# Optimization experiments

Hardware: AMD Instinct MI355X
Metric: run time of the kernel (lower is better)

## Reference

```python
import jax, jax.numpy as jnp
import numpy as np

IN_FEATURES = 512
NUM_CASES = 64
N_POINTS = 131072
HIDDEN = 512
OUT_FEATURES = 512


def _wn_linear(x, V, g, b):
    # torch weight_norm with dim=0 on Linear weight [out, in]: per-row norm over in-dim
    W = V * (g / jnp.linalg.norm(V, axis=1))[:, None]
    return x @ W.T + b


def _consolidative_matmul(mask, x):
    # group-by-caseID mean pooling expressed as masked matmul (matches torch forward)
    sel_sum = jnp.sum(mask, axis=-1, keepdims=True)
    sel_sum = jnp.maximum(sel_sum, 1.0)  # relu(s-1)+1 == max(s,1) for s>=0
    return (mask @ x) / sel_sum


def setup_inputs() -> dict:
    key = jax.random.key(0)
    ks = jax.random.split(key, 8)
    feat = jax.random.normal(ks[0], (N_POINTS, IN_FEATURES), dtype=jnp.float32)
    cid = jax.random.randint(ks[1], (N_POINTS, 1), 0, NUM_CASES).astype(jnp.float32)
    x = jnp.concatenate([feat, cid], axis=-1)  # [N, 513]
    s = 0.05
    V0 = jax.random.normal(ks[2], (HIDDEN, IN_FEATURES), dtype=jnp.float32) * s
    g0 = jnp.ones((HIDDEN,), dtype=jnp.float32)
    b0 = jnp.zeros((HIDDEN,), dtype=jnp.float32)
    V1 = jax.random.normal(ks[3], (HIDDEN, HIDDEN), dtype=jnp.float32) * s
    g1 = jnp.ones((HIDDEN,), dtype=jnp.float32)
    b1 = jnp.zeros((HIDDEN,), dtype=jnp.float32)
    Wf = jax.random.normal(ks[4], (OUT_FEATURES, HIDDEN), dtype=jnp.float32) * s
    bf = jnp.zeros((OUT_FEATURES,), dtype=jnp.float32)
    return {"x": x, "V0": V0, "g0": g0, "b0": b0,
            "V1": V1, "g1": g1, "b1": b1, "Wf": Wf, "bf": bf}


def reference(x, V0, g0, b0, V1, g1, b1, Wf, bf):
    feat = x[..., :IN_FEATURES]                    # [N, 512]
    cid = jax.lax.stop_gradient(x[..., IN_FEATURES:IN_FEATURES + 1])  # [N, 1]
    case_range = jnp.arange(NUM_CASES, dtype=x.dtype)[:, None]        # [C, 1]
    d = jnp.swapaxes(cid, -1, -2) - case_range     # [C, N]
    # Unit_function: 1 iff -0.5 < d < 0.5, else 0 (hard, zero-grad)
    mask = jnp.where((d > -0.5) & (d < 0.5), 1.0, 0.0).astype(x.dtype)
    mask = jax.lax.stop_gradient(mask)
    h = _consolidative_matmul(mask, feat)          # [C, 512] per-case mean
    h = jax.nn.silu(_wn_linear(h, V0, g0, b0))
    h = jax.nn.silu(_wn_linear(h, V1, g1, b1))
    h = h @ Wf.T + bf                              # final layer, identity activation
    out = jnp.swapaxes(mask, -1, -2) @ h           # scatter-back combine [N, 512]
    return out
```

## Files before the change

### kernel.cpp

```cpp
#include <hip/hip_runtime.h>
#include <math.h>

#define NPTS   131072
#define INF    512
#define ROWF   513
#define NCASE  64
#define HID    512
#define NB     256
#define CHUNK  512
#define SEG    16

__global__ __launch_bounds__(256)
void k_hist(const float* __restrict__ x, int* __restrict__ hist,
            int* __restrict__ cids) {
  __shared__ int h[NCASE];
  const int t = threadIdx.x;
  const int b = blockIdx.x;
  if (t < NCASE) h[t] = 0;
  __syncthreads();
  const int base = b * CHUNK;
  for (int i = t; i < CHUNK; i += 256) {
    float cf = x[(size_t)(base + i) * ROWF + INF];
    int c = (int)(cf + 0.5f);
    cids[base + i] = c;
    atomicAdd(&h[c], 1);
  }
  __syncthreads();
  if (t < NCASE) hist[b * NCASE + t] = h[t];
}

__global__ __launch_bounds__(64)
void k_scan(const int* __restrict__ hist, int* __restrict__ rel,
            int* __restrict__ base, int* __restrict__ cnt,
            float* __restrict__ cntf) {
  __shared__ int lcnt[NCASE];
  __shared__ int lbase[NCASE];
  const int c = threadIdx.x;
  int running = 0;
  for (int b = 0; b < NB; ++b) {
    rel[b * NCASE + c] = running;
    running += hist[b * NCASE + c];
  }
  lcnt[c] = running;
  cnt[c] = running;
  cntf[c] = (float)running;
  __syncthreads();
  if (c == 0) {
    int acc = 0;
    for (int i = 0; i < NCASE; ++i) { lbase[i] = acc; acc += lcnt[i]; }
  }
  __syncthreads();
  base[c] = lbase[c];
}

__global__ __launch_bounds__(64)
void k_build(const int* __restrict__ cids, const int* __restrict__ rel,
             const int* __restrict__ base, int* __restrict__ idxlist) {
  __shared__ int cidl[CHUNK];
  const int lane = threadIdx.x;
  const int b = blockIdx.x;
  for (int i = lane; i < CHUNK; i += 64) cidl[i] = cids[b * CHUNK + i];
  __syncthreads();
  int myoff = rel[b * NCASE + lane] + base[lane];
  int rank = 0;
  for (int i = 0; i < CHUNK; ++i) {
    if (cidl[i] == lane) { idxlist[myoff + rank] = b * CHUNK + i; ++rank; }
  }
}

__global__ __launch_bounds__(128)
void k_sum(const float* __restrict__ x, const int* __restrict__ idxlist,
           const int* __restrict__ base, const int* __restrict__ cnt,
           float* __restrict__ psum) {
  const int t = threadIdx.x;
  const int s = blockIdx.x;
  const int c = blockIdx.y;
  const int n = cnt[c];
  const int bs = base[c];
  int p0 = (s * n) / SEG;
  int p1 = ((s + 1) * n) / SEG;

  float a0 = 0.f, a1 = 0.f, a2 = 0.f, a3 = 0.f;
  int p = p0;
  for (; p + 4 <= p1; p += 4) {
    int i0 = __builtin_amdgcn_readfirstlane(idxlist[bs + p + 0]);
    int i1 = __builtin_amdgcn_readfirstlane(idxlist[bs + p + 1]);
    int i2 = __builtin_amdgcn_readfirstlane(idxlist[bs + p + 2]);
    int i3 = __builtin_amdgcn_readfirstlane(idxlist[bs + p + 3]);
    const float* r0 = x + (size_t)i0 * ROWF + t;
    const float* r1 = x + (size_t)i1 * ROWF + t;
    const float* r2 = x + (size_t)i2 * ROWF + t;
    const float* r3 = x + (size_t)i3 * ROWF + t;
    float v00 = r0[0], v01 = r0[128], v02 = r0[256], v03 = r0[384];
    float v10 = r1[0], v11 = r1[128], v12 = r1[256], v13 = r1[384];
    float v20 = r2[0], v21 = r2[128], v22 = r2[256], v23 = r2[384];
    float v30 = r3[0], v31 = r3[128], v32 = r3[256], v33 = r3[384];
    a0 += v00; a1 += v01; a2 += v02; a3 += v03;
    a0 += v10; a1 += v11; a2 += v12; a3 += v13;
    a0 += v20; a1 += v21; a2 += v22; a3 += v23;
    a0 += v30; a1 += v31; a2 += v32; a3 += v33;
  }
  for (; p < p1; ++p) {
    int i0 = __builtin_amdgcn_readfirstlane(idxlist[bs + p]);
    const float* r0 = x + (size_t)i0 * ROWF + t;
    a0 += r0[0]; a1 += r0[128]; a2 += r0[256]; a3 += r0[384];
  }
  float* od = psum + ((size_t)c * SEG + s) * HID;
  od[t] = a0; od[t + 128] = a1; od[t + 256] = a2; od[t + 384] = a3;
}

__global__ __launch_bounds__(512)
void k_h0(const float* __restrict__ psum, const float* __restrict__ cntf,
          float* __restrict__ h0) {
  const int c = blockIdx.x;
  const int f = threadIdx.x;
  float s = 0.f;
  for (int seg = 0; seg < SEG; ++seg) s += psum[((size_t)c * SEG + seg) * HID + f];
  h0[(size_t)c * HID + f] = s / fmaxf(cntf[c], 1.f);
}

__global__ __launch_bounds__(256)
void k_scale(const float* __restrict__ V, const float* __restrict__ g,
             float* __restrict__ scale, int K) {
  __shared__ float red[256];
  const int row = blockIdx.x;
  const int t   = threadIdx.x;
  const float* vr = V + (size_t)row * K;
  float s = 0.f;
  for (int k = t; k < K; k += 256) { float v = vr[k]; s += v * v; }
  red[t] = s;
  __syncthreads();
  for (int w = 128; w > 0; w >>= 1) {
    if (t < w) red[t] += red[t + w];
    __syncthreads();
  }
  if (t == 0) scale[row] = g[row] / sqrtf(red[0]);
}

template <bool SILU, bool SCALED>
__global__ __launch_bounds__(256)
void k_layer(const float* __restrict__ hin, const float* __restrict__ W,
             const float* __restrict__ scale, const float* __restrict__ bias,
             float* __restrict__ hout) {
  const int n = blockIdx.y;
  const int o = blockIdx.x * 256 + threadIdx.x;
  const float* hr = hin + (size_t)n * HID;
  const float* wr = W + (size_t)o * HID;
  float s0 = 0.f, s1 = 0.f, s2 = 0.f, s3 = 0.f;
  for (int k = 0; k < HID; k += 4) {
    s0 += hr[k + 0] * wr[k + 0];
    s1 += hr[k + 1] * wr[k + 1];
    s2 += hr[k + 2] * wr[k + 2];
    s3 += hr[k + 3] * wr[k + 3];
  }
  float s = (s0 + s1) + (s2 + s3);
  float y = SCALED ? (s * scale[o] + bias[o]) : (s + bias[o]);
  if (SILU) y = y / (1.f + expf(-y));
  hout[(size_t)n * HID + o] = y;
}

__global__ __launch_bounds__(256)
void k_scatter(const int* __restrict__ idxlist, const int* __restrict__ base,
               const int* __restrict__ cnt, const float* __restrict__ h3,
               float* __restrict__ out) {
  const int t = threadIdx.x;
  const int s = blockIdx.x;
  const int c = blockIdx.y;
  const int n = cnt[c];
  const int bs = base[c];
  int p0 = (s * n) / SEG;
  int p1 = ((s + 1) * n) / SEG;
  const int q = t & 127;
  const int which = t >> 7;
  float4 hv = ((const float4*)(h3 + (size_t)c * HID))[q];
  for (int p = p0 + which; p < p1; p += 2) {
    int idx = __builtin_amdgcn_readfirstlane(idxlist[bs + p]);
    ((float4*)(out + (size_t)idx * HID))[q] = hv;
  }
}

extern "C" void kernel_launch(void* const* d_in, const int* in_sizes, int n_in,
                              void* d_out, int out_size, void* d_ws, size_t ws_size,
                              hipStream_t stream) {
  const float* x  = (const float*)d_in[0];
  const float* V0 = (const float*)d_in[1];
  const float* g0 = (const float*)d_in[2];
  const float* b0 = (const float*)d_in[3];
  const float* V1 = (const float*)d_in[4];
  const float* g1 = (const float*)d_in[5];
  const float* b1 = (const float*)d_in[6];
  const float* Wf = (const float*)d_in[7];
  const float* bf = (const float*)d_in[8];
  float* out = (float*)d_out;
  float* ws  = (float*)d_ws;

  size_t off = 0;
  float* psum   = ws + off; off += (size_t)NCASE * SEG * HID;
  float* h0     = ws + off; off += NCASE * HID;
  float* h1     = ws + off; off += NCASE * HID;
  float* h2     = ws + off; off += NCASE * HID;
  float* h3     = ws + off; off += NCASE * HID;
  float* scale0 = ws + off; off += 512;
  float* scale1 = ws + off; off += 512;
  float* cntf   = ws + off; off += 64;
  int* iws = (int*)(ws + off);
  size_t ioff = 0;
  int* hist    = iws + ioff; ioff += NB * NCASE;
  int* rel     = iws + ioff; ioff += NB * NCASE;
  int* basec   = iws + ioff; ioff += NCASE;
  int* cnt     = iws + ioff; ioff += NCASE;
  int* cids    = iws + ioff; ioff += NPTS;
  int* idxlist = iws + ioff; ioff += NPTS;

  k_hist <<<dim3(NB), dim3(256), 0, stream>>>(x, hist, cids);
  k_scan <<<dim3(1), dim3(64), 0, stream>>>(hist, rel, basec, cnt, cntf);
  k_build<<<dim3(NB), dim3(64), 0, stream>>>(cids, rel, basec, idxlist);
  k_sum  <<<dim3(SEG, NCASE), dim3(128), 0, stream>>>(x, idxlist, basec, cnt, psum);
  k_h0   <<<dim3(NCASE), dim3(512), 0, stream>>>(psum, cntf, h0);
  k_scale<<<dim3(512), dim3(256), 0, stream>>>(V0, g0, scale0, HID);
  k_scale<<<dim3(512), dim3(256), 0, stream>>>(V1, g1, scale1, HID);
  k_layer<true,  true ><<<dim3(2, NCASE), dim3(256), 0, stream>>>(h0, V0, scale0, b0, h1);
  k_layer<true,  true ><<<dim3(2, NCASE), dim3(256), 0, stream>>>(h1, V1, scale1, b1, h2);
  k_layer<false, false><<<dim3(2, NCASE), dim3(256), 0, stream>>>(h2, Wf, nullptr, bf, h3);
  k_scatter<<<dim3(SEG, NCASE), dim3(256), 0, stream>>>(idxlist, basec, cnt, h3, out);
}
```

Measured before the change: 235.4 us.

## Parallelize scan, fuse reductions and scales, and scatter by point order

Replaces the serial single-block scan with a 64-block parallel Hillis-Steele scan over a transposed histogram. The per-case base offsets are recomputed with wave shuffles inside the consumer kernels. The two weight-norm scale kernels are merged into one, and the segment reduce (h0) is folded into the first layer kernel, which also stages its input row in shared memory. k_sum doubles its segment count and unrolls by 8. The scatter now walks points in order and writes contiguous output rows instead of gathering per case, aiming for coalesced stores. The aim is fewer launches, less serial latency and better memory access patterns. Costs are redundant per-block prefix sums and the segment reduction being repeated in both column blocks of layer 1.

```diff
diff --git a/kernel.cpp b/kernel.cpp
--- a/kernel.cpp
+++ b/kernel.cpp
@@ -8,7 +8,7 @@
 #define HID    512
 #define NB     256
 #define CHUNK  512
-#define SEG    16
+#define SEG    32
 
 __global__ __launch_bounds__(256)
 void k_hist(const float* __restrict__ x, int* __restrict__ hist,
@@ -26,42 +26,44 @@
     atomicAdd(&h[c], 1);
   }
   __syncthreads();
-  if (t < NCASE) hist[b * NCASE + t] = h[t];
-}
-
-__global__ __launch_bounds__(64)
+  if (t < NCASE) hist[t * NB + b] = h[t];
+}
+
+__global__ __launch_bounds__(256)
 void k_scan(const int* __restrict__ hist, int* __restrict__ rel,
-            int* __restrict__ base, int* __restrict__ cnt,
-            float* __restrict__ cntf) {
-  __shared__ int lcnt[NCASE];
-  __shared__ int lbase[NCASE];
-  const int c = threadIdx.x;
-  int running = 0;
-  for (int b = 0; b < NB; ++b) {
-    rel[b * NCASE + c] = running;
-    running += hist[b * NCASE + c];
-  }
-  lcnt[c] = running;
-  cnt[c] = running;
-  cntf[c] = (float)running;
-  __syncthreads();
-  if (c == 0) {
-    int acc = 0;
-    for (int i = 0; i < NCASE; ++i) { lbase[i] = acc; acc += lcnt[i]; }
-  }
-  __syncthreads();
-  base[c] = lbase[c];
+            int* __restrict__ cnt) {
+  __shared__ int buf[NB];
+  const int c = blockIdx.x;
+  const int t = threadIdx.x;
+  const int v = hist[c * NB + t];
+  buf[t] = v;
+  __syncthreads();
+  for (int d = 1; d < NB; d <<= 1) {
+    int u = (t >= d) ? buf[t - d] : 0;
+    __syncthreads();
+    buf[t] += u;
+    __syncthreads();
+  }
+  rel[t * NCASE + c] = buf[t] - v;
+  if (t == NB - 1) cnt[c] = buf[t];
 }
 
 __global__ __launch_bounds__(64)
 void k_build(const int* __restrict__ cids, const int* __restrict__ rel,
-             const int* __restrict__ base, int* __restrict__ idxlist) {
+             const int* __restrict__ cnt, int* __restrict__ idxlist) {
   __shared__ int cidl[CHUNK];
   const int lane = threadIdx.x;
   const int b = blockIdx.x;
   for (int i = lane; i < CHUNK; i += 64) cidl[i] = cids[b * CHUNK + i];
-  __syncthreads();
-  int myoff = rel[b * NCASE + lane] + base[lane];
+  int lv = cnt[lane];
+  int sc = lv;
+  for (int d = 1; d < 64; d <<= 1) {
+    int u = __shfl_up(sc, d, 64);
+    if (lane >= d) sc += u;
+  }
+  const int base = sc - lv;
+  __syncthreads();
+  int myoff = rel[b * NCASE + lane] + base;
   int rank = 0;
   for (int i = 0; i < CHUNK; ++i) {
     if (cidl[i] == lane) { idxlist[myoff + rank] = b * CHUNK + i; ++rank; }
@@ -70,112 +72,125 @@
 
 __global__ __launch_bounds__(128)
 void k_sum(const float* __restrict__ x, const int* __restrict__ idxlist,
-           const int* __restrict__ base, const int* __restrict__ cnt,
-           float* __restrict__ psum) {
+           const int* __restrict__ cnt, float* __restrict__ psum) {
   const int t = threadIdx.x;
   const int s = blockIdx.x;
   const int c = blockIdx.y;
-  const int n = cnt[c];
-  const int bs = base[c];
+  const int lane = t & 63;
+
+  int lv = cnt[lane];
+  int sc = lv;
+  for (int d = 1; d < 64; d <<= 1) {
+    int u = __shfl_up(sc, d, 64);
+    if (lane >= d) sc += u;
+  }
+  const int bs = __shfl(sc - lv, c, 64);
+  const int n  = __shfl(lv, c, 64);
+
   int p0 = (s * n) / SEG;
   int p1 = ((s + 1) * n) / SEG;
 
   float a0 = 0.f, a1 = 0.f, a2 = 0.f, a3 = 0.f;
   int p = p0;
-  for (; p + 4 <= p1; p += 4) {
-    int i0 = __builtin_amdgcn_readfirstlane(idxlist[bs + p + 0]);
-    int i1 = __builtin_amdgcn_readfirstlane(idxlist[bs + p + 1]);
-    int i2 = __builtin_amdgcn_readfirstlane(idxlist[bs + p + 2]);
-    int i3 = __builtin_amdgcn_readfirstlane(idxlist[bs + p + 3]);
-    const float* r0 = x + (size_t)i0 * ROWF + t;
-    const float* r1 = x + (size_t)i1 * ROWF + t;
-    const float* r2 = x + (size_t)i2 * ROWF + t;
-    const float* r3 = x + (size_t)i3 * ROWF + t;
-    float v00 = r0[0], v01 = r0[128], v02 = r0[256], v03 = r0[384];
-    float v10 = r1[0], v11 = r1[128], v12 = r1[256], v13 = r1[384];
-    float v20 = r2[0], v21 = r2[128], v22 = r2[256], v23 = r2[384];
-    float v30 = r3[0], v31 = r3[128], v32 = r3[256], v33 = r3[384];
-    a0 += v00; a1 += v01; a2 += v02; a3 += v03;
-    a0 += v10; a1 += v11; a2 += v12; a3 += v13;
-    a0 += v20; a1 += v21; a2 += v22; a3 += v23;
-    a0 += v30; a1 += v31; a2 += v32; a3 += v33;
+  for (; p + 8 <= p1; p += 8) {
+    int idx[8];
+    #pragma unroll
+    for (int j = 0; j < 8; ++j)
+      idx[j] = __builtin_amdgcn_readfirstlane(idxlist[bs + p + j]);
+    float v[8][4];
+    #pragma unroll
+    for (int j = 0; j < 8; ++j) {
+      const float* r = x + (size_t)idx[j] * ROWF + t;
+      v[j][0] = r[0]; v[j][1] = r[128]; v[j][2] = r[256]; v[j][3] = r[384];
+    }
+    #pragma unroll
+    for (int j = 0; j < 8; ++j) {
+      a0 += v[j][0]; a1 += v[j][1]; a2 += v[j][2]; a3 += v[j][3];
+    }
   }
   for (; p < p1; ++p) {
     int i0 = __builtin_amdgcn_readfirstlane(idxlist[bs + p]);
-    const float* r0 = x + (size_t)i0 * ROWF + t;
-    a0 += r0[0]; a1 += r0[128]; a2 += r0[256]; a3 += r0[384];
+    const float* r = x + (size_t)i0 * ROWF + t;
+    a0 += r[0]; a1 += r[128]; a2 += r[256]; a3 += r[384];
   }
   float* od = psum + ((size_t)c * SEG + s) * HID;
   od[t] = a0; od[t + 128] = a1; od[t + 256] = a2; od[t + 384] = a3;
 }
 
-__global__ __launch_bounds__(512)
-void k_h0(const float* __restrict__ psum, const float* __restrict__ cntf,
-          float* __restrict__ h0) {
-  const int c = blockIdx.x;
-  const int f = threadIdx.x;
-  float s = 0.f;
-  for (int seg = 0; seg < SEG; ++seg) s += psum[((size_t)c * SEG + seg) * HID + f];
-  h0[(size_t)c * HID + f] = s / fmaxf(cntf[c], 1.f);
-}
-
-__global__ __launch_bounds__(256)
-void k_scale(const float* __restrict__ V, const float* __restrict__ g,
-             float* __restrict__ scale, int K) {
+__global__ __launch_bounds__(256)
+void k_scale2(const float* __restrict__ V0, const float* __restrict__ g0,
+              const float* __restrict__ V1, const float* __restrict__ g1,
+              float* __restrict__ scale0, float* __restrict__ scale1) {
   __shared__ float red[256];
   const int row = blockIdx.x;
   const int t   = threadIdx.x;
-  const float* vr = V + (size_t)row * K;
+  const bool first = row < 512;
+  const int r = first ? row : row - 512;
+  const float* vr = (first ? V0 : V1) + (size_t)r * HID;
   float s = 0.f;
-  for (int k = t; k < K; k += 256) { float v = vr[k]; s += v * v; }
+  for (int k = t; k < HID; k += 256) { float v = vr[k]; s += v * v; }
   red[t] = s;
   __syncthreads();
   for (int w = 128; w > 0; w >>= 1) {
     if (t < w) red[t] += red[t + w];
     __syncthreads();
   }
-  if (t == 0) scale[row] = g[row] / sqrtf(red[0]);
-}
-
-template <bool SILU, bool SCALED>
+  if (t == 0) {
+    float g = first ? g0[r] : g1[r];
+    (first ? scale0 : scale1)[r] = g / sqrtf(red[0]);
+  }
+}
+
+template <bool SILU, bool SCALED, bool REDUCE>
 __global__ __launch_bounds__(256)
 void k_layer(const float* __restrict__ hin, const float* __restrict__ W,
              const float* __restrict__ scale, const float* __restrict__ bias,
-             float* __restrict__ hout) {
+             const int* __restrict__ cnt, float* __restrict__ hout) {
+  __shared__ float hrow[HID];
   const int n = blockIdx.y;
-  const int o = blockIdx.x * 256 + threadIdx.x;
-  const float* hr = hin + (size_t)n * HID;
+  const int t = threadIdx.x;
+  const int o = blockIdx.x * 256 + t;
+  if (REDUCE) {
+    float inv = 1.f / fmaxf((float)cnt[n], 1.f);
+    for (int f = t; f < HID; f += 256) {
+      float s = 0.f;
+      for (int seg = 0; seg < SEG; ++seg)
+        s += hin[((size_t)n * SEG + seg) * HID + f];
+      hrow[f] = s * inv;
+    }
+  } else {
+    for (int f = t; f < HID; f += 256) hrow[f] = hin[(size_t)n * HID + f];
+  }
+  __syncthreads();
   const float* wr = W + (size_t)o * HID;
   float s0 = 0.f, s1 = 0.f, s2 = 0.f, s3 = 0.f;
   for (int k = 0; k < HID; k += 4) {
-    s0 += hr[k + 0] * wr[k + 0];
-    s1 += hr[k + 1] * wr[k + 1];
-    s2 += hr[k + 2] * wr[k + 2];
-    s3 += hr[k + 3] * wr[k + 3];
-  }
-  float s = (s0 + s1) + (s2 + s3);
-  float y = SCALED ? (s * scale[o] + bias[o]) : (s + bias[o]);
+    float4 h4 = *(const float4*)&hrow[k];
+    float4 w4 = *(const float4*)&wr[k];
+    s0 += h4.x * w4.x; s1 += h4.y * w4.y;
+    s2 += h4.z * w4.z; s3 += h4.w * w4.w;
+  }
+  float sdot = (s0 + s1) + (s2 + s3);
+  float y = SCALED ? (sdot * scale[o] + bias[o]) : (sdot + bias[o]);
   if (SILU) y = y / (1.f + expf(-y));
   hout[(size_t)n * HID + o] = y;
 }
 
 __global__ __launch_bounds__(256)
-void k_scatter(const int* __restrict__ idxlist, const int* __restrict__ base,
-               const int* __restrict__ cnt, const float* __restrict__ h3,
+void k_scatter(const int* __restrict__ cids, const float* __restrict__ h3,
                float* __restrict__ out) {
-  const int t = threadIdx.x;
-  const int s = blockIdx.x;
-  const int c = blockIdx.y;
-  const int n = cnt[c];
-  const int bs = base[c];
-  int p0 = (s * n) / SEG;
-  int p1 = ((s + 1) * n) / SEG;
+  __shared__ int cl[64];
+  const int t = threadIdx.x;
   const int q = t & 127;
-  const int which = t >> 7;
-  float4 hv = ((const float4*)(h3 + (size_t)c * HID))[q];
-  for (int p = p0 + which; p < p1; p += 2) {
-    int idx = __builtin_amdgcn_readfirstlane(idxlist[bs + p]);
-    ((float4*)(out + (size_t)idx * HID))[q] = hv;
+  const int half = t >> 7;
+  const int base = blockIdx.x * 64;
+  if (t < 64) cl[t] = cids[base + t];
+  __syncthreads();
+  #pragma unroll 4
+  for (int p = half; p < 64; p += 2) {
+    int c = cl[p];
+    float4 hv = ((const float4*)(h3 + (size_t)c * HID))[q];
+    ((float4*)(out + (size_t)(base + p) * HID))[q] = hv;
   }
 }
 
@@ -196,31 +211,26 @@
 
   size_t off = 0;
   float* psum   = ws + off; off += (size_t)NCASE * SEG * HID;
-  float* h0     = ws + off; off += NCASE * HID;
   float* h1     = ws + off; off += NCASE * HID;
   float* h2     = ws + off; off += NCASE * HID;
   float* h3     = ws + off; off += NCASE * HID;
   float* scale0 = ws + off; off += 512;
   float* scale1 = ws + off; off += 512;
-  float* cntf   = ws + off; off += 64;
   int* iws = (int*)(ws + off);
   size_t ioff = 0;
-  int* hist    = iws + ioff; ioff += NB * NCASE;
+  int* hist    = iws + ioff; ioff += NCASE * NB;
   int* rel     = iws + ioff; ioff += NB * NCASE;
-  int* basec   = iws + ioff; ioff += NCASE;
   int* cnt     = iws + ioff; ioff += NCASE;
   int* cids    = iws + ioff; ioff += NPTS;
   int* idxlist = iws + ioff; ioff += NPTS;
 
-  k_hist <<<dim3(NB), dim3(256), 0, stream>>>(x, hist, cids);
-  k_scan <<<dim3(1), dim3(64), 0, stream>>>(hist, rel, basec, cnt, cntf);
-  k_build<<<dim3(NB), dim3(64), 0, stream>>>(cids, rel, basec, idxlist);
-  k_sum  <<<dim3(SEG, NCASE), dim3(128), 0, stream>>>(x, idxlist, basec, cnt, psum);
-  k_h0   <<<dim3(NCASE), dim3(512), 0, stream>>>(psum, cntf, h0);
-  k_scale<<<dim3(512), dim3(256), 0, stream>>>(V0, g0, scale0, HID);
-  k_scale<<<dim3(512), dim3(256), 0, stream>>>(V1, g1, scale1, HID);
-  k_layer<true,  true ><<<dim3(2, NCASE), dim3(256), 0, stream>>>(h0, V0, scale0, b0, h1);
-  k_layer<true,  true ><<<dim3(2, NCASE), dim3(256), 0, stream>>>(h1, V1, scale1, b1, h2);
-  k_layer<false, false><<<dim3(2, NCASE), dim3(256), 0, stream>>>(h2, Wf, nullptr, bf, h3);
-  k_scatter<<<dim3(SEG, NCASE), dim3(256), 0, stream>>>(idxlist, basec, cnt, h3, out);
-}
+  k_scale2<<<dim3(1024), dim3(256), 0, stream>>>(V0, g0, V1, g1, scale0, scale1);
+  k_hist  <<<dim3(NB), dim3(256), 0, stream>>>(x, hist, cids);
+  k_scan  <<<dim3(NCASE), dim3(NB), 0, stream>>>(hist, rel, cnt);
+  k_build <<<dim3(NB), dim3(64), 0, stream>>>(cids, rel, cnt, idxlist);
+  k_sum   <<<dim3(SEG, NCASE), dim3(128), 0, stream>>>(x, idxlist, cnt, psum);
+  k_layer<true,  true,  true ><<<dim3(2, NCASE), dim3(256), 0, stream>>>(psum, V0, scale0, b0, cnt, h1);
+  k_layer<true,  true,  false><<<dim3(2, NCASE), dim3(256), 0, stream>>>(h1,   V1, scale1, b1, cnt, h2);
+  k_layer<false, false, false><<<dim3(2, NCASE), dim3(256), 0, stream>>>(h2,   Wf, nullptr, bf, cnt, h3);
+  k_scatter<<<dim3(NPTS / 64), dim3(256), 0, stream>>>(cids, h3, out);
+}
```

New measurement: 233.2 us. No clear change (-0.9%).
